# Performance work log

Measured on AMD Instinct MI355X. Metric: run time of the kernel, lower is better.

The kernel has to match this reference:

```python
import jax, jax.numpy as jnp
import numpy as np

B, D, Q = 1024, 512, 32768


def setup_inputs() -> dict:
    key = jax.random.key(0)
    kx, kq = jax.random.split(key)
    x = jax.random.normal(kx, (B, D), dtype=jnp.float32)
    queue_prev = jax.random.normal(kq, (Q, D), dtype=jnp.float32)
    return {"x": x, "queue_prev": queue_prev}


def reference(x, queue_prev):
    # Queue.forward: enqueue x, keep last queue_size rows (queue assumed full)
    q_size = queue_prev.shape[0]
    queue = jnp.concatenate([queue_prev, x], axis=0)[-q_size:]  # [Q, D]

    # euclidean metric == torch.cdist(x, queue): [B, Q]
    d2 = (
        jnp.sum(x * x, axis=-1, keepdims=True)
        + jnp.sum(queue * queue, axis=-1)[None, :]
        - 2.0 * (x @ queue.T)
    )
    dist = jnp.sqrt(jnp.maximum(d2, 0.0))

    # topk(-dist, 2): two smallest distances; take the 2nd (skip self-match)
    _, indices = jax.lax.top_k(-dist, 2)  # [B, 2]
    nn_idx = indices[:, -1]  # [B]
    return queue[nn_idx]  # [B, D]
```

## Files before the change

### kernel.cpp

```cpp
#include <hip/hip_runtime.h>
#include <hip/hip_bf16.h>
#include <hip/hip_fp16.h>

#define B_N 1024
#define D_N 512
#define Q_N 32768
#define QSHIFT (Q_N - B_N)

#define KP 1024
#define KL 1536
#define BKx 32
#define NKB (KL / BKx)
#define NCH 256

typedef __attribute__((ext_vector_type(8))) _Float16 half8;
typedef __attribute__((ext_vector_type(4))) float f32x4;

__device__ __forceinline__ void top2_update(float d, int j,
                                            float& d1, int& i1, float& d2, int& i2) {
  if (d < d1 || (d == d1 && j < i1)) { d2 = d1; i2 = i1; d1 = d; i1 = j; }
  else if (d < d2 || (d == d2 && j < i2)) { d2 = d; i2 = j; }
}

__global__ __launch_bounds__(256) void prep_kernel(const float* __restrict__ x,
                                                   const float* __restrict__ qp,
                                                   _Float16* __restrict__ Qpk,
                                                   _Float16* __restrict__ Apk,
                                                   float* __restrict__ q2n) {
  const int row  = blockIdx.x * 4 + (threadIdx.x >> 6);
  const int lane = threadIdx.x & 63;
  const bool is_q = row < Q_N;
  const float* src;
  _Float16* dst;
  if (is_q) {
    src = (row < QSHIFT) ? qp + (size_t)(row + B_N) * D_N
                         : x  + (size_t)(row - QSHIFT) * D_N;
    dst = Qpk + (size_t)row * KP;
  } else {
    src = x + (size_t)(row - Q_N) * D_N;
    dst = Apk + (size_t)(row - Q_N) * KP;
  }
  const float4* p = (const float4*)src;
  float4 a = p[lane * 2], b = p[lane * 2 + 1];
  float v[8] = {a.x, a.y, a.z, a.w, b.x, b.y, b.z, b.w};
  _Float16 hi[8] __attribute__((aligned(16)));
  _Float16 lo[8] __attribute__((aligned(16)));
  float s = 0.0f;
  #pragma unroll
  for (int u = 0; u < 8; ++u) {
    s += v[u] * v[u];
    hi[u] = (_Float16)v[u];
    lo[u] = (_Float16)(v[u] - (float)hi[u]);
  }
  *(uint4*)(dst + lane * 8)       = *(const uint4*)hi;
  *(uint4*)(dst + 512 + lane * 8) = *(const uint4*)lo;
  if (is_q) {
    #pragma unroll
    for (int off = 32; off; off >>= 1) s += __shfl_down(s, off);
    if (lane == 0) q2n[row] = s;
  }
}

__global__ __launch_bounds__(256, 3) void nn_mfma(const _Float16* __restrict__ Apk,
                                                  const _Float16* __restrict__ Qpk,
                                                  const float* __restrict__ q2n,
                                                  float4* __restrict__ partial) {
  __shared__ __align__(128) char smem[32768];

  const int bid  = blockIdx.x;
  const int work = (bid & 7) * 256 + (bid >> 3);
  const int chunk = work >> 3;
  const int mblk  = work & 7;
  const int n0 = chunk * 128;
  const int i0 = mblk * 128;

  const int t = threadIdx.x;
  const int lane = t & 63;
  const int wv = t >> 6;
  const int wm = (wv >> 1) * 64;
  const int wn = (wv & 1) * 64;
  const int srow = lane >> 2;
  const int gcol = (((lane & 3) ^ ((lane >> 3) & 3)) * 8);
  const int fr = lane & 15;
  const int fg = lane >> 4;
  const int rswz = (fg ^ ((fr >> 1) & 3)) * 16;

  f32x4 acc[4][4] = {};

  auto stage = [&](int buf, int kb) {
    int ka, kq;
    if (kb < 16)      { ka = kb * 32;              kq = ka; }
    else if (kb < 32) { ka = 512 + (kb - 16) * 32; kq = (kb - 16) * 32; }
    else              { ka = (kb - 32) * 32;       kq = 512 + (kb - 32) * 32; }
    char* base = smem + buf * 16384;
    #pragma unroll
    for (int c = 0; c < 2; ++c) {
      const int r = c * 64 + wv * 16;
      const _Float16* ga = Apk + (size_t)(i0 + r + srow) * KP + ka + gcol;
      const _Float16* gb = Qpk + (size_t)(n0 + r + srow) * KP + kq + gcol;
      __builtin_amdgcn_global_load_lds(
          (const __attribute__((address_space(1))) void*)ga,
          (__attribute__((address_space(3))) void*)(base + r * 64), 16, 0, 0);
      __builtin_amdgcn_global_load_lds(
          (const __attribute__((address_space(1))) void*)gb,
          (__attribute__((address_space(3))) void*)(base + 8192 + r * 64), 16, 0, 0);
    }
  };

  stage(0, 0);
  asm volatile("s_waitcnt vmcnt(0)" ::: "memory");
  __syncthreads();

  int cur = 0;
  for (int kb = 0; kb < NKB; ++kb) {
    if (kb + 1 < NKB) stage(cur ^ 1, kb + 1);

    const char* base = smem + cur * 16384;
    half8 af[4], bf[4];
    #pragma unroll
    for (int mi = 0; mi < 4; ++mi)
      af[mi] = *(const half8*)(base + (wm + mi * 16 + fr) * 64 + rswz);
    #pragma unroll
    for (int ni = 0; ni < 4; ++ni)
      bf[ni] = *(const half8*)(base + 8192 + (wn + ni * 16 + fr) * 64 + rswz);
    #pragma unroll
    for (int mi = 0; mi < 4; ++mi)
      #pragma unroll
      for (int ni = 0; ni < 4; ++ni)
        acc[mi][ni] = __builtin_amdgcn_mfma_f32_16x16x32_f16(af[mi], bf[ni], acc[mi][ni], 0, 0, 0);

    asm volatile("s_waitcnt vmcnt(0)" ::: "memory");
    __syncthreads();
    cur ^= 1;
  }

  float4 (*red)[8] = (float4(*)[8])smem;

  float q2v[4];
  #pragma unroll
  for (int ni = 0; ni < 4; ++ni) q2v[ni] = q2n[n0 + wn + ni * 16 + fr];

  #pragma unroll
  for (int mi = 0; mi < 4; ++mi) {
    #pragma unroll
    for (int r = 0; r < 4; ++r) {
      float d1 = 3.4e38f, d2v = 3.4e38f;
      int   i1 = 0x7fffffff, i2v = 0x7fffffff;
      #pragma unroll
      for (int ni = 0; ni < 4; ++ni) {
        const float d = q2v[ni] - 2.0f * acc[mi][ni][r];
        top2_update(d, n0 + wn + ni * 16 + fr, d1, i1, d2v, i2v);
      }
      #pragma unroll
      for (int off = 1; off <= 2; off <<= 1) {
        float e1 = __shfl_xor(d1, off);  int j1 = __shfl_xor(i1, off);
        float e2 = __shfl_xor(d2v, off); int j2 = __shfl_xor(i2v, off);
        top2_update(e1, j1, d1, i1, d2v, i2v);
        top2_update(e2, j2, d1, i1, d2v, i2v);
      }
      if ((lane & 3) == 0)
        red[wm + mi * 16 + fg * 4 + r][(wv & 1) * 4 + (fr >> 2)] =
            make_float4(d1, __int_as_float(i1), d2v, __int_as_float(i2v));
    }
  }
  __syncthreads();

  {
    const int row = t >> 1, part = t & 1;
    float d1 = 3.4e38f, d2 = 3.4e38f;
    int   i1 = 0x7fffffff, i2 = 0x7fffffff;
    #pragma unroll
    for (int u = 0; u < 4; ++u) {
      float4 v = red[row][part * 4 + u];
      top2_update(v.x, __float_as_int(v.y), d1, i1, d2, i2);
      top2_update(v.z, __float_as_int(v.w), d1, i1, d2, i2);
    }
    float e1 = __shfl_xor(d1, 1); int j1 = __shfl_xor(i1, 1);
    float e2 = __shfl_xor(d2, 1); int j2 = __shfl_xor(i2, 1);
    top2_update(e1, j1, d1, i1, d2, i2);
    top2_update(e2, j2, d1, i1, d2, i2);
    if (part == 0)
      partial[(size_t)(i0 + row) * NCH + chunk] =
          make_float4(d1, __int_as_float(i1), d2, __int_as_float(i2));
  }
}

__global__ __launch_bounds__(128) void nn_merge256(const float* __restrict__ x,
                                                   const float* __restrict__ qp,
                                                   const float4* __restrict__ partial,
                                                   float* __restrict__ out) {
  const int row = blockIdx.x;
  const int t   = threadIdx.x;
  __shared__ int s_nn;
  if (t < 64) {
    float d1 = 3.4e38f, d2 = 3.4e38f;
    int   i1 = 0x7fffffff, i2 = 0x7fffffff;
    #pragma unroll
    for (int u = 0; u < 4; ++u) {
      float4 v = partial[(size_t)row * NCH + u * 64 + t];
      top2_update(v.x, __float_as_int(v.y), d1, i1, d2, i2);
      top2_update(v.z, __float_as_int(v.w), d1, i1, d2, i2);
    }
    #pragma unroll
    for (int off = 1; off < 64; off <<= 1) {
      float e1 = __shfl_xor(d1, off); int j1 = __shfl_xor(i1, off);
      float e2 = __shfl_xor(d2, off); int j2 = __shfl_xor(i2, off);
      top2_update(e1, j1, d1, i1, d2, i2);
      top2_update(e2, j2, d1, i1, d2, i2);
    }
    if (t == 0) s_nn = i2;
  }
  __syncthreads();
  const int nn = s_nn;
  const float* src = (nn < QSHIFT) ? qp + (size_t)(nn + B_N) * D_N
                                   : x  + (size_t)(nn - QSHIFT) * D_N;
  ((float4*)(out + (size_t)row * D_N))[t] = ((const float4*)src)[t];
}

#define TM 64
#define TN 64
#define BKf 16
#define JCHUNK 512
#define NCHUNK (Q_N / JCHUNK)

__global__ __launch_bounds__(256) void qnorm_kernel(const float* __restrict__ x,
                                                    const float* __restrict__ qp,
                                                    float* __restrict__ q2) {
  const int row  = blockIdx.x * 4 + (threadIdx.x >> 6);
  const int lane = threadIdx.x & 63;
  const float* src = (row < QSHIFT) ? (qp + (size_t)(row + B_N) * D_N)
                                    : (x  + (size_t)(row - QSHIFT) * D_N);
  const float4* p = (const float4*)src;
  float4 a = p[lane];
  float4 b = p[lane + 64];
  float s = a.x*a.x + a.y*a.y + a.z*a.z + a.w*a.w
          + b.x*b.x + b.y*b.y + b.z*b.z + b.w*b.w;
  #pragma unroll
  for (int off = 32; off; off >>= 1) s += __shfl_down(s, off);
  if (lane == 0) q2[row] = s;
}

__global__ __launch_bounds__(256) void nn_main(const float* __restrict__ x,
                                               const float* __restrict__ qp,
                                               const float* __restrict__ q2,
                                               float4* __restrict__ partial) {
  __shared__ float As[BKf][TM];
  __shared__ float Bs[BKf][TN];
  __shared__ float4 red[TM][16];
  const int chunk = blockIdx.x;
  const int i0    = blockIdx.y * TM;
  const int t     = threadIdx.x;
  const int tx    = t & 15;
  const int ty    = t >> 4;
  const int lrow  = t >> 2;
  const int kp    = t & 3;
  float d1[4], d2v[4];
  int   i1[4], i2v[4];
  #pragma unroll
  for (int m = 0; m < 4; ++m) { d1[m] = 3.4e38f; d2v[m] = 3.4e38f; i1[m] = 0x7fffffff; i2v[m] = 0x7fffffff; }
  const int j_base = chunk * JCHUNK;
  for (int jt = 0; jt < JCHUNK / TN; ++jt) {
    const int j0 = j_base + jt * TN;
    float acc[4][4] = {};
    const int jr = j0 + lrow;
    const float* bsrc = (jr < QSHIFT) ? (qp + (size_t)(jr + B_N) * D_N)
                                      : (x  + (size_t)(jr - QSHIFT) * D_N);
    const float* asrc = x + (size_t)(i0 + lrow) * D_N;
    for (int k0 = 0; k0 < D_N; k0 += BKf) {
      float4 a4 = *(const float4*)&asrc[k0 + kp * 4];
      float4 b4 = *(const float4*)&bsrc[k0 + kp * 4];
      __syncthreads();
      As[kp*4+0][lrow] = a4.x; As[kp*4+1][lrow] = a4.y;
      As[kp*4+2][lrow] = a4.z; As[kp*4+3][lrow] = a4.w;
      Bs[kp*4+0][lrow] = b4.x; Bs[kp*4+1][lrow] = b4.y;
      Bs[kp*4+2][lrow] = b4.z; Bs[kp*4+3][lrow] = b4.w;
      __syncthreads();
      #pragma unroll
      for (int kk = 0; kk < BKf; ++kk) {
        float4 av = *(const float4*)&As[kk][ty * 4];
        float4 bv = *(const float4*)&Bs[kk][tx * 4];
        float am[4] = {av.x, av.y, av.z, av.w};
        float bm[4] = {bv.x, bv.y, bv.z, bv.w};
        #pragma unroll
        for (int m = 0; m < 4; ++m)
          #pragma unroll
          for (int c = 0; c < 4; ++c)
            acc[m][c] = fmaf(am[m], bm[c], acc[m][c]);
      }
    }
    #pragma unroll
    for (int m = 0; m < 4; ++m)
      #pragma unroll
      for (int c = 0; c < 4; ++c) {
        const int j = j0 + tx * 4 + c;
        const float d = q2[j] - 2.0f * acc[m][c];
        top2_update(d, j, d1[m], i1[m], d2v[m], i2v[m]);
      }
  }
  __syncthreads();
  #pragma unroll
  for (int m = 0; m < 4; ++m)
    red[ty * 4 + m][tx] = make_float4(d1[m], __int_as_float(i1[m]),
                                      d2v[m], __int_as_float(i2v[m]));
  __syncthreads();
  if (t < TM) {
    float bd1 = 3.4e38f, bd2 = 3.4e38f;
    int   bi1 = 0x7fffffff, bi2 = 0x7fffffff;
    #pragma unroll
    for (int u = 0; u < 16; ++u) {
      float4 v = red[t][u];
      top2_update(v.x, __float_as_int(v.y), bd1, bi1, bd2, bi2);
      top2_update(v.z, __float_as_int(v.w), bd1, bi1, bd2, bi2);
    }
    partial[(size_t)(i0 + t) * NCHUNK + chunk] =
        make_float4(bd1, __int_as_float(bi1), bd2, __int_as_float(bi2));
  }
}

__global__ __launch_bounds__(128) void nn_merge(const float* __restrict__ x,
                                                const float* __restrict__ qp,
                                                const float4* __restrict__ partial,
                                                float* __restrict__ out) {
  const int row = blockIdx.x;
  const int t   = threadIdx.x;
  __shared__ int s_nn;
  if (t < 64) {
    float4 v = partial[(size_t)row * NCHUNK + t];
    float d1 = v.x, d2 = v.z;
    int   i1 = __float_as_int(v.y), i2 = __float_as_int(v.w);
    #pragma unroll
    for (int off = 1; off < 64; off <<= 1) {
      float e1 = __shfl_xor(d1, off); int j1 = __shfl_xor(i1, off);
      float e2 = __shfl_xor(d2, off); int j2 = __shfl_xor(i2, off);
      top2_update(e1, j1, d1, i1, d2, i2);
      top2_update(e2, j2, d1, i1, d2, i2);
    }
    if (t == 0) s_nn = i2;
  }
  __syncthreads();
  const int nn = s_nn;
  const float* src = (nn < QSHIFT) ? (qp + (size_t)(nn + B_N) * D_N)
                                   : (x  + (size_t)(nn - QSHIFT) * D_N);
  *(float4*)&out[(size_t)row * D_N + t * 4] = *(const float4*)&src[t * 4];
}

extern "C" void kernel_launch(void* const* d_in, const int* in_sizes, int n_in,
                              void* d_out, int out_size, void* d_ws, size_t ws_size,
                              hipStream_t stream) {
  const float* x  = (const float*)d_in[0];
  const float* qp = (const float*)d_in[1];
  float* out = (float*)d_out;

  const size_t off_apk = 0;
  const size_t off_qpk = off_apk + (size_t)B_N * KP * sizeof(_Float16);
  const size_t off_q2n = off_qpk + (size_t)Q_N * KP * sizeof(_Float16);
  const size_t off_par = off_q2n + (size_t)Q_N * sizeof(float);
  const size_t need    = off_par + (size_t)B_N * NCH * sizeof(float4);

  if (ws_size >= need) {
    _Float16* Apk = (_Float16*)((char*)d_ws + off_apk);
    _Float16* Qpk = (_Float16*)((char*)d_ws + off_qpk);
    float*    q2n = (float*)((char*)d_ws + off_q2n);
    float4*   par = (float4*)((char*)d_ws + off_par);
    prep_kernel<<<(Q_N + B_N) / 4, 256, 0, stream>>>(x, qp, Qpk, Apk, q2n);
    nn_mfma<<<2048, 256, 0, stream>>>(Apk, Qpk, q2n, par);
    nn_merge256<<<B_N, 128, 0, stream>>>(x, qp, par, out);
  } else {
    float*  q2      = (float*)d_ws;
    float4* partial = (float4*)((char*)d_ws + Q_N * sizeof(float));
    qnorm_kernel<<<Q_N / 4, 256, 0, stream>>>(x, qp, q2);
    nn_main<<<dim3(NCHUNK, B_N / TM), 256, 0, stream>>>(x, qp, q2, partial);
    nn_merge<<<B_N, 128, 0, stream>>>(x, qp, partial, out);
  }
}
```

Before: 422.1 us.

## Stage hi and lo fp16 splits together per k-step with larger LDS buffers

New measurement: 448.9 us. +6.4%, slower.

```diff
diff --git a/kernel.cpp b/kernel.cpp
--- a/kernel.cpp
+++ b/kernel.cpp
@@ -8,9 +8,7 @@
 #define QSHIFT (Q_N - B_N)
 
 #define KP 1024
-#define KL 1536
-#define BKx 32
-#define NKB (KL / BKx)
+#define NSTEP 16
 #define NCH 256
 
 typedef __attribute__((ext_vector_type(8))) _Float16 half8;
@@ -61,11 +59,11 @@
   }
 }
 
-__global__ __launch_bounds__(256, 3) void nn_mfma(const _Float16* __restrict__ Apk,
+__global__ __launch_bounds__(256, 2) void nn_mfma(const _Float16* __restrict__ Apk,
                                                   const _Float16* __restrict__ Qpk,
                                                   const float* __restrict__ q2n,
                                                   float4* __restrict__ partial) {
-  __shared__ __align__(128) char smem[32768];
+  __shared__ __align__(128) char smem[65536];
 
   const int bid  = blockIdx.x;
   const int work = (bid & 7) * 256 + (bid >> 3);
@@ -87,50 +85,61 @@
 
   f32x4 acc[4][4] = {};
 
+  auto gld = [](const _Float16* g, char* l) {
+    __builtin_amdgcn_global_load_lds(
+        (const __attribute__((address_space(1))) void*)g,
+        (__attribute__((address_space(3))) void*)l, 16, 0, 0);
+  };
+
   auto stage = [&](int buf, int kb) {
-    int ka, kq;
-    if (kb < 16)      { ka = kb * 32;              kq = ka; }
-    else if (kb < 32) { ka = 512 + (kb - 16) * 32; kq = (kb - 16) * 32; }
-    else              { ka = (kb - 32) * 32;       kq = 512 + (kb - 32) * 32; }
-    char* base = smem + buf * 16384;
-    #pragma unroll
-    for (int c = 0; c < 2; ++c) {
-      const int r = c * 64 + wv * 16;
-      const _Float16* ga = Apk + (size_t)(i0 + r + srow) * KP + ka + gcol;
-      const _Float16* gb = Qpk + (size_t)(n0 + r + srow) * KP + kq + gcol;
-      __builtin_amdgcn_global_load_lds(
-          (const __attribute__((address_space(1))) void*)ga,
-          (__attribute__((address_space(3))) void*)(base + r * 64), 16, 0, 0);
-      __builtin_amdgcn_global_load_lds(
-          (const __attribute__((address_space(1))) void*)gb,
-          (__attribute__((address_space(3))) void*)(base + 8192 + r * 64), 16, 0, 0);
+    const int k0 = kb * 32;
+    char* base = smem + buf * 32768;
+    #pragma unroll
+    for (int h = 0; h < 2; ++h) {
+      const int r = wv * 32 + h * 16;
+      const _Float16* ga = Apk + (size_t)(i0 + r + srow) * KP + k0 + gcol;
+      const _Float16* gb = Qpk + (size_t)(n0 + r + srow) * KP + k0 + gcol;
+      gld(ga,        base +          r * 64);
+      gld(ga + 512,  base +  8192 + r * 64);
+      gld(gb,        base + 16384 + r * 64);
+      gld(gb + 512,  base + 24576 + r * 64);
     }
   };
 
   stage(0, 0);
   asm volatile("s_waitcnt vmcnt(0)" ::: "memory");
-  __syncthreads();
+  __builtin_amdgcn_s_barrier();
 
   int cur = 0;
-  for (int kb = 0; kb < NKB; ++kb) {
-    if (kb + 1 < NKB) stage(cur ^ 1, kb + 1);
-
-    const char* base = smem + cur * 16384;
-    half8 af[4], bf[4];
+  for (int kb = 0; kb < NSTEP; ++kb) {
+    if (kb + 1 < NSTEP) stage(cur ^ 1, kb + 1);
+
+    const char* base = smem + cur * 32768;
+    half8 afh[4], afl[4], bfh[4], bfl[4];
+    #pragma unroll
+    for (int mi = 0; mi < 4; ++mi) {
+      afh[mi] = *(const half8*)(base +          (wm + mi * 16 + fr) * 64 + rswz);
+      afl[mi] = *(const half8*)(base +  8192 + (wm + mi * 16 + fr) * 64 + rswz);
+    }
+    #pragma unroll
+    for (int ni = 0; ni < 4; ++ni) {
+      bfh[ni] = *(const half8*)(base + 16384 + (wn + ni * 16 + fr) * 64 + rswz);
+      bfl[ni] = *(const half8*)(base + 24576 + (wn + ni * 16 + fr) * 64 + rswz);
+    }
+
+    __builtin_amdgcn_s_setprio(1);
     #pragma unroll
     for (int mi = 0; mi < 4; ++mi)
-      af[mi] = *(const half8*)(base + (wm + mi * 16 + fr) * 64 + rswz);
-    #pragma unroll
-    for (int ni = 0; ni < 4; ++ni)
-      bf[ni] = *(const half8*)(base + 8192 + (wn + ni * 16 + fr) * 64 + rswz);
-    #pragma unroll
-    for (int mi = 0; mi < 4; ++mi)
-      #pragma unroll
-      for (int ni = 0; ni < 4; ++ni)
-        acc[mi][ni] = __builtin_amdgcn_mfma_f32_16x16x32_f16(af[mi], bf[ni], acc[mi][ni], 0, 0, 0);
+      #pragma unroll
+      for (int ni = 0; ni < 4; ++ni) {
+        acc[mi][ni] = __builtin_amdgcn_mfma_f32_16x16x32_f16(afh[mi], bfh[ni], acc[mi][ni], 0, 0, 0);
+        acc[mi][ni] = __builtin_amdgcn_mfma_f32_16x16x32_f16(afl[mi], bfh[ni], acc[mi][ni], 0, 0, 0);
+        acc[mi][ni] = __builtin_amdgcn_mfma_f32_16x16x32_f16(afh[mi], bfl[ni], acc[mi][ni], 0, 0, 0);
+      }
+    __builtin_amdgcn_s_setprio(0);
 
     asm volatile("s_waitcnt vmcnt(0)" ::: "memory");
-    __syncthreads();
+    __builtin_amdgcn_s_barrier();
     cur ^= 1;
   }
 
```
